# Kernel tuning notes

Hardware: AMD Instinct MI355X
Metric: run time of the kernel (lower is better)

The kernel has to match this reference:

```python
import jax, jax.numpy as jnp
import numpy as np

N = 100000
E = 1600000
K = 2  # KProp steps


def setup_inputs() -> dict:
    key = jax.random.key(0)
    ks = jax.random.split(key, 8)
    x = jax.random.normal(ks[0], (N, 64), dtype=jnp.float32)
    edge_index = jax.random.randint(ks[1], (2, E), 0, N, dtype=jnp.int32)
    s = 1.0 / np.sqrt(64)
    W2l = jax.random.normal(ks[2], (64, 64), dtype=jnp.float32) * s
    W2r = jax.random.normal(ks[3], (64, 64), dtype=jnp.float32) * s
    b2 = jnp.zeros((64,), dtype=jnp.float32)
    W3l = jax.random.normal(ks[4], (64, 16), dtype=jnp.float32) * s
    W3r = jax.random.normal(ks[5], (64, 16), dtype=jnp.float32) * s
    b3 = jnp.zeros((16,), dtype=jnp.float32)
    return {"x": x, "edge_index": edge_index, "W2l": W2l, "W2r": W2r,
            "b2": b2, "W3l": W3l, "W3r": W3r, "b3": b3}


def reference(x, edge_index, W2l, W2r, b2, W3l, W3r, b3):
    dst, src = edge_index[0], edge_index[1]  # adj_t[i,j]: edge j -> i
    ones = jnp.ones((E,), dtype=x.dtype)
    deg = jax.ops.segment_sum(ones, dst, num_segments=N)  # in-degree
    dinv = jnp.where(deg > 0, jax.lax.rsqrt(jnp.maximum(deg, 1.0)), 0.0)
    w = dinv[dst] * dinv[src]  # gcn_norm weights (no self-loops in norm)

    # KProp: K steps of (D^-1/2 A D^-1/2 + I) @ h  (set_diag adds unit diag)
    h = x
    for _ in range(K):
        h = jax.ops.segment_sum(w[:, None] * h[src], dst, num_segments=N) + h

    degm = jnp.maximum(deg, 1.0)[:, None]

    # SAGEConv 1: mean-neighbor aggregate + root weight
    agg = jax.ops.segment_sum(h[src], dst, num_segments=N) / degm
    h = agg @ W2l + h @ W2r + b2
    h = jax.nn.selu(h)

    # SAGEConv 2
    agg = jax.ops.segment_sum(h[src], dst, num_segments=N) / degm
    h = agg @ W3l + h @ W3r + b3
    return jax.nn.softmax(h, axis=1)
```

## Files before the change

kernel.cpp:

```cpp
#include <hip/hip_runtime.h>
#include <hip/hip_bf16.h>

#define NNODES 100000
#define NEDGES 1600000
#define NC 25
#define CAP1 68000
#define NBUCK 391
#define BCAP 4800
#define SPLIT_TILE 4096
#define NSPLIT ((NEDGES + SPLIT_TILE - 1) / SPLIT_TILE)
#define T2TILES 17
#define NTILES (NNODES / 16)

typedef short short8 __attribute__((ext_vector_type(8)));
typedef unsigned short ushx8 __attribute__((ext_vector_type(8)));
typedef float floatx4 __attribute__((ext_vector_type(4)));

__device__ __forceinline__ unsigned short f2b(float f) {
    unsigned u = __float_as_uint(f);
    u += 0x7fffu + ((u >> 16) & 1u);
    return (unsigned short)(u >> 16);
}

__device__ __forceinline__ void acc8(float* a, ushx8 u) {
#pragma unroll
    for (int i = 0; i < 8; ++i)
        a[i] += __uint_as_float((unsigned)u[i] << 16);
}

__device__ __forceinline__ void acc8s(float* a, ushx8 u, float s) {
#pragma unroll
    for (int i = 0; i < 8; ++i)
        a[i] = fmaf(s, __uint_as_float((unsigned)u[i] << 16), a[i]);
}

__global__ __launch_bounds__(256) void split1_kernel(
    const int* __restrict__ dst, const int* __restrict__ src,
    int* __restrict__ gcur1, unsigned* __restrict__ cpairs) {
    __shared__ int lhist[NC];
    __shared__ int lstart[NC];
    __shared__ int ldst[SPLIT_TILE];
    int t = threadIdx.x;
    if (t < NC) lhist[t] = 0;
    __syncthreads();
    int base = blockIdx.x * SPLIT_TILE;
    int n = min(SPLIT_TILE, NEDGES - base);
    for (int i = t; i < n; i += 256) {
        int d = dst[base + i];
        ldst[i] = d;
        atomicAdd(&lhist[d >> 12], 1);
    }
    __syncthreads();
    if (t < NC) {
        int c = lhist[t];
        lstart[t] = (c > 0) ? atomicAdd(&gcur1[t], c) : 0;
        lhist[t] = 0;
    }
    __syncthreads();
    for (int i = t; i < n; i += 256) {
        int d = ldst[i];
        int k = d >> 12;
        int s = src[base + i];
        int pos = lstart[k] + atomicAdd(&lhist[k], 1);
        cpairs[(size_t)k * CAP1 + pos] = ((unsigned)s << 12) | (unsigned)(d & 4095);
    }
}

__global__ __launch_bounds__(256) void split2_kernel(
    const unsigned* __restrict__ cpairs, const int* __restrict__ gcur1,
    int* __restrict__ gcur2, unsigned* __restrict__ fpairs) {
    int c = blockIdx.x / T2TILES;
    int tile = blockIdx.x % T2TILES;
    int cnt = gcur1[c];
    int base = tile * 4096;
    if (base >= cnt) return;
    int n = min(4096, cnt - base);
    __shared__ unsigned stash[4096];
    __shared__ int lhist[16];
    __shared__ int lstart[16];
    int t = threadIdx.x;
    if (t < 16) lhist[t] = 0;
    __syncthreads();
    const unsigned* pb = cpairs + (size_t)c * CAP1 + base;
    for (int i = t; i < n; i += 256) {
        unsigned p = pb[i];
        stash[i] = p;
        atomicAdd(&lhist[(p >> 8) & 15], 1);
    }
    __syncthreads();
    if (t < 16) {
        int cc = lhist[t];
        lstart[t] = (cc > 0) ? atomicAdd(&gcur2[c * 16 + t], cc) : 0;
        lhist[t] = 0;
    }
    __syncthreads();
    for (int i = t; i < n; i += 256) {
        unsigned p = stash[i];
        int f = (p >> 8) & 15;
        int pos = lstart[f] + atomicAdd(&lhist[f], 1);
        fpairs[(size_t)(c * 16 + f) * BCAP + pos] = ((p >> 12) << 8) | (p & 255u);
    }
}

__global__ __launch_bounds__(256) void finalize_kernel(
    const unsigned* __restrict__ fpairs, const int* __restrict__ gcur2,
    const float* __restrict__ x,
    int* __restrict__ col, int* __restrict__ deg, int* __restrict__ rowoff,
    float* __restrict__ dinv, unsigned short* __restrict__ g0b) {
    __shared__ int ldeg[256];
    __shared__ int lcur[256];
    __shared__ float ldi[256];
    __shared__ int lsc[256];
    __shared__ int bb[NBUCK + 1];
    int k = blockIdx.x;
    int t = threadIdx.x;
    int a2 = (2 * t < NBUCK) ? gcur2[2 * t] : 0;
    int b2v = (2 * t + 1 < NBUCK) ? gcur2[2 * t + 1] : 0;
    int ts = a2 + b2v;
    lsc[t] = ts;
    __syncthreads();
    for (int s = 1; s < 256; s <<= 1) {
        int v = (t >= s) ? lsc[t - s] : 0;
        __syncthreads();
        lsc[t] += v;
        __syncthreads();
    }
    int excl2 = lsc[t] - ts;
    if (2 * t < NBUCK) bb[2 * t] = excl2;
    if (2 * t + 1 < NBUCK) bb[2 * t + 1] = excl2 + a2;
    ldeg[t] = 0;
    __syncthreads();
    int node0 = k << 8;
    int ncount = min(256, NNODES - node0);
    int base = bb[k];
    int count = gcur2[k];
    const unsigned* pb = fpairs + (size_t)k * BCAP;
    for (int i = t; i < count; i += 256) {
        atomicAdd(&ldeg[pb[i] & 255], 1);
    }
    __syncthreads();
    int a = ldeg[t];
    lsc[t] = a;
    __syncthreads();
    for (int s = 1; s < 256; s <<= 1) {
        int v = (t >= s) ? lsc[t - s] : 0;
        __syncthreads();
        lsc[t] += v;
        __syncthreads();
    }
    int excl = lsc[t] - a;
    lcur[t] = base + excl;
    if (t < ncount) {
        int n0 = node0 + t;
        rowoff[n0] = base + excl;
        deg[n0] = a;
        float di = (a > 0) ? rsqrtf((float)a) : 0.0f;
        ldi[t] = di;
        dinv[n0] = di;
    }
    __syncthreads();
    for (int i = t; i < count; i += 256) {
        unsigned p = pb[i];
        int dl = (int)(p & 255u);
        int s = (int)(p >> 8);
        int pos = atomicAdd(&lcur[dl], 1);
        col[pos] = s;
    }
    const float4* x4 = (const float4*)x;
    int f4count = ncount * 16;
    int b4 = node0 * 16;
    for (int j = t; j < f4count; j += 256) {
        float di = ldi[j >> 4];
        float4 v = x4[b4 + j];
        ushort4 u;
        u.x = f2b(di * v.x); u.y = f2b(di * v.y);
        u.z = f2b(di * v.z); u.w = f2b(di * v.w);
        *(ushort4*)(g0b + (size_t)(b4 + j) * 4) = u;
    }
}

template <int MODE>
__global__ __launch_bounds__(256) void gatherw_kernel(
    const unsigned short* __restrict__ vin, const float* __restrict__ hinf,
    const unsigned short* __restrict__ hinb,
    unsigned short* __restrict__ out0,
    const int* __restrict__ rowoff, const int* __restrict__ deg,
    const int* __restrict__ col, const float* __restrict__ dinv) {
    int node = blockIdx.x * 4 + (threadIdx.x >> 6);
    int lane = threadIdx.x & 63;
    int sub = lane & 7;
    int g = lane >> 3;
    int beg = rowoff[node];
    int dg = deg[node];
    int end = beg + dg;
    float af[8] = {0.f, 0.f, 0.f, 0.f, 0.f, 0.f, 0.f, 0.f};
    float bf[8] = {0.f, 0.f, 0.f, 0.f, 0.f, 0.f, 0.f, 0.f};
    int e = beg + g;
    for (; e + 8 < end; e += 16) {
        int c0 = col[e];
        int c1 = col[e + 8];
        ushx8 u0 = *(const ushx8*)(vin + (size_t)c0 * 64 + sub * 8);
        ushx8 u1 = *(const ushx8*)(vin + (size_t)c1 * 64 + sub * 8);
        if (MODE == 1) {
            float d0 = dinv[c0];
            float d1 = dinv[c1];
            acc8s(af, u0, d0);
            acc8s(bf, u1, d1);
        } else {
            acc8(af, u0);
            acc8(bf, u1);
        }
    }
    if (e < end) {
        int c0 = col[e];
        ushx8 u0 = *(const ushx8*)(vin + (size_t)c0 * 64 + sub * 8);
        if (MODE == 1) {
            float d0 = dinv[c0];
            acc8s(af, u0, d0);
        } else {
            acc8(af, u0);
        }
    }
#pragma unroll
    for (int i = 0; i < 8; ++i) {
        float v = af[i] + bf[i];
        v += __shfl_xor(v, 8);
        v += __shfl_xor(v, 16);
        v += __shfl_xor(v, 32);
        af[i] = v;
    }
    if (lane < 8) {
        size_t off = (size_t)node * 64 + lane * 8;
        ushx8 uh;
        if (MODE <= 1) {
            float di = dinv[node];
            float hv[8];
            if (MODE == 0) {
                float4 h0 = *(const float4*)(hinf + off);
                float4 h1 = *(const float4*)(hinf + off + 4);
                hv[0] = h0.x; hv[1] = h0.y; hv[2] = h0.z; hv[3] = h0.w;
                hv[4] = h1.x; hv[5] = h1.y; hv[6] = h1.z; hv[7] = h1.w;
            } else {
                ushx8 u = *(const ushx8*)(hinb + off);
#pragma unroll
                for (int i = 0; i < 8; ++i) hv[i] = __uint_as_float((unsigned)u[i] << 16);
            }
#pragma unroll
            for (int i = 0; i < 8; ++i) uh[i] = f2b(hv[i] + di * af[i]);
        } else {
            float r = 1.0f / (float)(dg > 0 ? dg : 1);
#pragma unroll
            for (int i = 0; i < 8; ++i) uh[i] = f2b(af[i] * r);
        }
        *(ushx8*)(out0 + off) = uh;
    }
}

__global__ __launch_bounds__(256) void dense1_mfma(
    const unsigned short* __restrict__ aggb, const unsigned short* __restrict__ hb,
    unsigned short* __restrict__ h3b,
    const float* __restrict__ W2l, const float* __restrict__ W2r,
    const float* __restrict__ b2) {
    __shared__ unsigned short Wt[64 * 144];
    int t = threadIdx.x;
    for (int idx = t; idx < 128 * 64; idx += 256) {
        int k = idx >> 6, j = idx & 63;
        float v = (k < 64) ? W2l[k * 64 + j] : W2r[(k - 64) * 64 + j];
        Wt[j * 144 + k] = f2b(v);
    }
    __syncthreads();
    int wib = t >> 6, lane = t & 63;
    int tile = blockIdx.x * 4 + wib;
    if (tile >= NTILES) return;
    int node0 = tile * 16;
    int jj = lane & 15, kg = lane >> 4;
    short8 bfrag[4][4];
#pragma unroll
    for (int nt = 0; nt < 4; ++nt)
#pragma unroll
        for (int s = 0; s < 4; ++s)
            bfrag[nt][s] = *(const short8*)&Wt[(nt * 16 + jj) * 144 + s * 32 + kg * 8];
    int arow = node0 + jj;
    const unsigned short* ap = aggb + (size_t)arow * 64 + kg * 8;
    const unsigned short* hp = hb + (size_t)arow * 64 + kg * 8;
    short8 afrag[4];
    afrag[0] = *(const short8*)ap;
    afrag[1] = *(const short8*)(ap + 32);
    afrag[2] = *(const short8*)hp;
    afrag[3] = *(const short8*)(hp + 32);
    const float lam = 1.0507009873554804934193349852946f;
    const float alp = 1.6732632423543772848170429916717f;
#pragma unroll
    for (int nt = 0; nt < 4; ++nt) {
        floatx4 acc = {0.f, 0.f, 0.f, 0.f};
#pragma unroll
        for (int s = 0; s < 4; ++s)
            acc = __builtin_amdgcn_mfma_f32_16x16x32_bf16(afrag[s], bfrag[nt][s], acc, 0, 0, 0);
        float bias = b2[nt * 16 + jj];
#pragma unroll
        for (int r = 0; r < 4; ++r) {
            float v = acc[r] + bias;
            float o = (v > 0.0f) ? lam * v : lam * alp * expm1f(v);
            int node = node0 + kg * 4 + r;
            h3b[(size_t)node * 64 + nt * 16 + jj] = f2b(o);
        }
    }
}

__global__ __launch_bounds__(256) void dense2_mfma(
    const unsigned short* __restrict__ aggb, const unsigned short* __restrict__ hb,
    float* __restrict__ out,
    const float* __restrict__ W3l, const float* __restrict__ W3r,
    const float* __restrict__ b3) {
    __shared__ unsigned short Wt[16 * 144];
    int t = threadIdx.x;
    for (int idx = t; idx < 128 * 16; idx += 256) {
        int k = idx >> 4, j = idx & 15;
        float v = (k < 64) ? W3l[k * 16 + j] : W3r[(k - 64) * 16 + j];
        Wt[j * 144 + k] = f2b(v);
    }
    __syncthreads();
    int wib = t >> 6, lane = t & 63;
    int tile = blockIdx.x * 4 + wib;
    if (tile >= NTILES) return;
    int node0 = tile * 16;
    int jj = lane & 15, kg = lane >> 4;
    short8 bfrag[4];
#pragma unroll
    for (int s = 0; s < 4; ++s)
        bfrag[s] = *(const short8*)&Wt[jj * 144 + s * 32 + kg * 8];
    int arow = node0 + jj;
    const unsigned short* ap = aggb + (size_t)arow * 64 + kg * 8;
    const unsigned short* hp = hb + (size_t)arow * 64 + kg * 8;
    short8 afrag[4];
    afrag[0] = *(const short8*)ap;
    afrag[1] = *(const short8*)(ap + 32);
    afrag[2] = *(const short8*)hp;
    afrag[3] = *(const short8*)(hp + 32);
    floatx4 acc = {0.f, 0.f, 0.f, 0.f};
#pragma unroll
    for (int s = 0; s < 4; ++s)
        acc = __builtin_amdgcn_mfma_f32_16x16x32_bf16(afrag[s], bfrag[s], acc, 0, 0, 0);
    float bias = b3[jj];
#pragma unroll
    for (int r = 0; r < 4; ++r) {
        float v = acc[r] + bias;
        float m = v;
        m = fmaxf(m, __shfl_xor(m, 1));
        m = fmaxf(m, __shfl_xor(m, 2));
        m = fmaxf(m, __shfl_xor(m, 4));
        m = fmaxf(m, __shfl_xor(m, 8));
        float ex = expf(v - m);
        float s2 = ex;
        s2 += __shfl_xor(s2, 1);
        s2 += __shfl_xor(s2, 2);
        s2 += __shfl_xor(s2, 4);
        s2 += __shfl_xor(s2, 8);
        int node = node0 + kg * 4 + r;
        out[(size_t)node * 16 + jj] = ex / s2;
    }
}

extern "C" void kernel_launch(void* const* d_in, const int* in_sizes, int n_in,
                              void* d_out, int out_size, void* d_ws, size_t ws_size,
                              hipStream_t stream) {
    const float* x   = (const float*)d_in[0];
    const int*   ei  = (const int*)d_in[1];
    const float* W2l = (const float*)d_in[2];
    const float* W2r = (const float*)d_in[3];
    const float* b2  = (const float*)d_in[4];
    const float* W3l = (const float*)d_in[5];
    const float* W3r = (const float*)d_in[6];
    const float* b3  = (const float*)d_in[7];
    float* out = (float*)d_out;

    const int* dst = ei;
    const int* src = ei + NEDGES;

    char* ws = (char*)d_ws;
    unsigned short* B0 = (unsigned short*)ws; ws += (size_t)NNODES * 64 * 2;
    unsigned short* B1 = (unsigned short*)ws; ws += (size_t)NNODES * 64 * 2;
    unsigned short* B2 = (unsigned short*)ws; ws += (size_t)NNODES * 64 * 2;
    int*      col     = (int*)ws;      ws += (size_t)NEDGES * 4;
    int*      deg     = (int*)ws;      ws += (size_t)NNODES * 4;
    int*      rowoff  = (int*)ws;      ws += (size_t)NNODES * 4;
    float*    dinv    = (float*)ws;    ws += (size_t)NNODES * 4;
    int*      gcur1   = (int*)ws;      ws += NC * 4;
    int*      gcur2   = (int*)ws;      ws += NBUCK * 4;

    unsigned* cpairs = (unsigned*)B1;
    unsigned* fpairs = (unsigned*)B2;
    unsigned short* h1b = B1;
    unsigned short* h2b = B0;
    unsigned short* h3b = B1;

    hipMemsetAsync(gcur1, 0, (NC + NBUCK) * 4, stream);

    split1_kernel<<<NSPLIT, 256, 0, stream>>>(dst, src, gcur1, cpairs);
    split2_kernel<<<NC * T2TILES, 256, 0, stream>>>(cpairs, gcur1, gcur2, fpairs);
    finalize_kernel<<<NBUCK, 256, 0, stream>>>(fpairs, gcur2, x,
                                               col, deg, rowoff, dinv, B0);

    int nblk = NNODES / 4;
    int ndense = (NTILES + 3) / 4;
    gatherw_kernel<0><<<nblk, 256, 0, stream>>>(B0, x, nullptr, h1b, rowoff, deg, col, dinv);
    gatherw_kernel<1><<<nblk, 256, 0, stream>>>(h1b, nullptr, h1b, h2b, rowoff, deg, col, dinv);
    gatherw_kernel<2><<<nblk, 256, 0, stream>>>(h2b, nullptr, nullptr, B2, rowoff, deg, col, dinv);
    dense1_mfma<<<ndense, 256, 0, stream>>>(B2, h2b, h3b, W2l, W2r, b2);
    gatherw_kernel<2><<<nblk, 256, 0, stream>>>(h3b, nullptr, nullptr, B2, rowoff, deg, col, dinv);
    dense2_mfma<<<ndense, 256, 0, stream>>>(B2, h3b, out, W3l, W3r, b3);
}
```

Measured before the change: 324.7 us.

## Merge two-pass edge bucketing into a single 391-bucket split pass

Replaces the two-level radix split (25 coarse buckets, then 16 fine buckets each) with one kernel that histograms edges straight into 391 buckets of 256 destination nodes and scatters packed (src, dst-low-byte) pairs into a dedicated fpairs buffer. This removes one kernel launch and a full read and write of the intermediate pair array. In exchange each block keeps a larger shared histogram, issues many more global atomics for bucket offsets, and scatters its writes across many more destinations, so writes are less coalesced. It also allocates a separate workspace region for fpairs instead of aliasing B2.

```diff
diff --git a/kernel.cpp b/kernel.cpp
--- a/kernel.cpp
+++ b/kernel.cpp
@@ -3,13 +3,10 @@
 
 #define NNODES 100000
 #define NEDGES 1600000
-#define NC 25
-#define CAP1 68000
 #define NBUCK 391
 #define BCAP 4800
 #define SPLIT_TILE 4096
 #define NSPLIT ((NEDGES + SPLIT_TILE - 1) / SPLIT_TILE)
-#define T2TILES 17
 #define NTILES (NNODES / 16)
 
 typedef short short8 __attribute__((ext_vector_type(8)));
@@ -34,71 +31,32 @@
         a[i] = fmaf(s, __uint_as_float((unsigned)u[i] << 16), a[i]);
 }
 
-__global__ __launch_bounds__(256) void split1_kernel(
+__global__ __launch_bounds__(256) void split_kernel(
     const int* __restrict__ dst, const int* __restrict__ src,
-    int* __restrict__ gcur1, unsigned* __restrict__ cpairs) {
-    __shared__ int lhist[NC];
-    __shared__ int lstart[NC];
-    __shared__ int ldst[SPLIT_TILE];
+    int* __restrict__ gcur, unsigned* __restrict__ fpairs) {
+    __shared__ int lhist[NBUCK];
+    __shared__ int lstart[NBUCK];
     int t = threadIdx.x;
-    if (t < NC) lhist[t] = 0;
+    for (int i = t; i < NBUCK; i += 256) lhist[i] = 0;
     __syncthreads();
     int base = blockIdx.x * SPLIT_TILE;
     int n = min(SPLIT_TILE, NEDGES - base);
     for (int i = t; i < n; i += 256) {
+        atomicAdd(&lhist[dst[base + i] >> 8], 1);
+    }
+    __syncthreads();
+    for (int i = t; i < NBUCK; i += 256) {
+        int c = lhist[i];
+        lstart[i] = (c > 0) ? atomicAdd(&gcur[i], c) : 0;
+        lhist[i] = 0;
+    }
+    __syncthreads();
+    for (int i = t; i < n; i += 256) {
         int d = dst[base + i];
-        ldst[i] = d;
-        atomicAdd(&lhist[d >> 12], 1);
-    }
-    __syncthreads();
-    if (t < NC) {
-        int c = lhist[t];
-        lstart[t] = (c > 0) ? atomicAdd(&gcur1[t], c) : 0;
-        lhist[t] = 0;
-    }
-    __syncthreads();
-    for (int i = t; i < n; i += 256) {
-        int d = ldst[i];
-        int k = d >> 12;
         int s = src[base + i];
+        int k = d >> 8;
         int pos = lstart[k] + atomicAdd(&lhist[k], 1);
-        cpairs[(size_t)k * CAP1 + pos] = ((unsigned)s << 12) | (unsigned)(d & 4095);
-    }
-}
-
-__global__ __launch_bounds__(256) void split2_kernel(
-    const unsigned* __restrict__ cpairs, const int* __restrict__ gcur1,
-    int* __restrict__ gcur2, unsigned* __restrict__ fpairs) {
-    int c = blockIdx.x / T2TILES;
-    int tile = blockIdx.x % T2TILES;
-    int cnt = gcur1[c];
-    int base = tile * 4096;
-    if (base >= cnt) return;
-    int n = min(4096, cnt - base);
-    __shared__ unsigned stash[4096];
-    __shared__ int lhist[16];
-    __shared__ int lstart[16];
-    int t = threadIdx.x;
-    if (t < 16) lhist[t] = 0;
-    __syncthreads();
-    const unsigned* pb = cpairs + (size_t)c * CAP1 + base;
-    for (int i = t; i < n; i += 256) {
-        unsigned p = pb[i];
-        stash[i] = p;
-        atomicAdd(&lhist[(p >> 8) & 15], 1);
-    }
-    __syncthreads();
-    if (t < 16) {
-        int cc = lhist[t];
-        lstart[t] = (cc > 0) ? atomicAdd(&gcur2[c * 16 + t], cc) : 0;
-        lhist[t] = 0;
-    }
-    __syncthreads();
-    for (int i = t; i < n; i += 256) {
-        unsigned p = stash[i];
-        int f = (p >> 8) & 15;
-        int pos = lstart[f] + atomicAdd(&lhist[f], 1);
-        fpairs[(size_t)(c * 16 + f) * BCAP + pos] = ((p >> 12) << 8) | (p & 255u);
+        fpairs[(size_t)k * BCAP + pos] = ((unsigned)s << 8) | (unsigned)(d & 255);
     }
 }
 
@@ -381,24 +339,21 @@
     unsigned short* B0 = (unsigned short*)ws; ws += (size_t)NNODES * 64 * 2;
     unsigned short* B1 = (unsigned short*)ws; ws += (size_t)NNODES * 64 * 2;
     unsigned short* B2 = (unsigned short*)ws; ws += (size_t)NNODES * 64 * 2;
+    unsigned* fpairs  = (unsigned*)ws; ws += (size_t)NBUCK * BCAP * 4;
     int*      col     = (int*)ws;      ws += (size_t)NEDGES * 4;
     int*      deg     = (int*)ws;      ws += (size_t)NNODES * 4;
     int*      rowoff  = (int*)ws;      ws += (size_t)NNODES * 4;
     float*    dinv    = (float*)ws;    ws += (size_t)NNODES * 4;
-    int*      gcur1   = (int*)ws;      ws += NC * 4;
-    int*      gcur2   = (int*)ws;      ws += NBUCK * 4;
-
-    unsigned* cpairs = (unsigned*)B1;
-    unsigned* fpairs = (unsigned*)B2;
+    int*      gcur    = (int*)ws;      ws += NBUCK * 4;
+
     unsigned short* h1b = B1;
     unsigned short* h2b = B0;
     unsigned short* h3b = B1;
 
-    hipMemsetAsync(gcur1, 0, (NC + NBUCK) * 4, stream);
-
-    split1_kernel<<<NSPLIT, 256, 0, stream>>>(dst, src, gcur1, cpairs);
-    split2_kernel<<<NC * T2TILES, 256, 0, stream>>>(cpairs, gcur1, gcur2, fpairs);
-    finalize_kernel<<<NBUCK, 256, 0, stream>>>(fpairs, gcur2, x,
+    hipMemsetAsync(gcur, 0, NBUCK * 4, stream);
+
+    split_kernel<<<NSPLIT, 256, 0, stream>>>(dst, src, gcur, fpairs);
+    finalize_kernel<<<NBUCK, 256, 0, stream>>>(fpairs, gcur, x,
                                                col, deg, rowoff, dinv, B0);
 
     int nblk = NNODES / 4;
```

After: 324.2 us. No clear change (-0.2%).
